# Optimization experiments

Measured on AMD Instinct MI355X. Metric: run time of the kernel, lower is better.

## Reference

```python
import jax, jax.numpy as jnp
import numpy as np

B, L, H, NH, HD, IT = 16, 512, 256, 8, 32, 2
NEG = -9e15


def _ln(x, g, b):
    m = x.mean(-1, keepdims=True)
    v = ((x - m) ** 2).mean(-1, keepdims=True)
    return (x - m) / jnp.sqrt(v + 1e-5) * g + b


def setup_inputs() -> dict:
    key = jax.random.key(0)
    ks = jax.random.split(key, 12)

    def nrm(k, shape, fan_in):
        return jax.random.normal(k, shape, dtype=jnp.float32) / np.float32(np.sqrt(fan_in))

    return {
        "data": jax.random.normal(ks[0], (B, L, H), jnp.float32),
        "gat_WQ_w": nrm(ks[1], (NH, H, H), H),
        "gat_WQ_b": jnp.zeros((NH, H), jnp.float32),
        "gat_a1": nrm(ks[2], (NH, 3 * H), 3 * H),
        "gat_a2": nrm(ks[3], (NH, 3 * H), 3 * H),
        "gat_fc_w": nrm(ks[4], (NH, 3 * H, HD), 3 * H),
        "gat_fc_b": jnp.zeros((NH, HD), jnp.float32),
        "norm_g": jnp.ones((IT, H), jnp.float32),
        "norm_b": jnp.zeros((IT, H), jnp.float32),
        "sq_w": nrm(ks[5], (IT, NH * HD, H), H),
        "sq_b": jnp.zeros((IT, NH * HD), jnp.float32),
        "sk_w": nrm(ks[6], (IT, NH * HD, H), H),
        "sk_b": jnp.zeros((IT, NH * HD), jnp.float32),
        "so_w": nrm(ks[7], (IT, H, NH * HD), NH * HD),
        "so_b": jnp.zeros((IT, H), jnp.float32),
        "fc_w": nrm(ks[8], (NH * HD, H), NH * HD),
        "fc_b": jnp.zeros((H,), jnp.float32),
        "mask": jax.random.randint(ks[9], (B, L), 0, 2, jnp.int32),
        "edge_matrix": jax.random.randint(ks[10], (B, L, L), 0, 2, jnp.int32),
    }


def _gat_head(xn, ax, adj_pos, Wq, bq, a1, a2, Fw, Fb):
    # xn: [B,L,H] normalized nodes; ax: [B,L,2H] interleaved (r_embs, relay)
    h = jnp.concatenate([xn @ Wq.T + bq, ax], axis=-1)  # [B,L,3H]
    # decomposed a^T [h_i ; h_j] = a1.h_i + a2.h_j  (avoids O(N^2*6H) concat)
    ei = h @ a1  # [B,L]
    ej = h @ a2  # [B,L]
    e = jax.nn.leaky_relu(ei[:, :, None] + ej[:, None, :], 0.2)  # [B,L,L]
    att = jax.nn.softmax(jnp.where(adj_pos, e, NEG), axis=2)
    hp = jnp.einsum('bij,bjd->bid', att, h)  # [B,L,3H]
    return jax.nn.elu(hp @ Fw + Fb)  # [B,L,HD]


def _forward(data, gat_WQ_w, gat_WQ_b, gat_a1, gat_a2, gat_fc_w, gat_fc_b,
             norm_g, norm_b, sq_w, sq_b, sk_w, sk_b, so_w, so_b, fc_w, fc_b,
             mask, edge_matrix):
    pad = mask == 0                                   # True at padding positions
    smask = jnp.concatenate([jnp.zeros((B, 1), bool), pad], axis=1)  # [B,L+1]
    adj_pos = edge_matrix > 0
    nodes = data                                      # [B,L,H]
    relay = data.mean(axis=1)                         # [B,H]
    gat = jax.vmap(_gat_head, in_axes=(None, None, None, 0, 0, 0, 0, 0, 0))
    scale = np.float32(1.0 / np.sqrt(HD))

    for i in range(IT):
        xn = _ln(nodes, norm_g[i], norm_b[i])
        # torch views [B,H,2,L] as [B,2H,L]: features interleave (r_embs, relay)
        ax = jnp.stack([data, jnp.broadcast_to(relay[:, None, :], (B, L, H))],
                       axis=-1).reshape(B, L, 2 * H)
        heads = gat(xn, ax, adj_pos, gat_WQ_w, gat_WQ_b, gat_a1, gat_a2,
                    gat_fc_w, gat_fc_b)               # [NH,B,L,HD]
        temp = jnp.transpose(heads, (1, 2, 0, 3)).reshape(B, L, NH * HD)
        nodes = nodes + jax.nn.leaky_relu(temp @ fc_w + fc_b, 0.01)
        # star attention (MSA2); note original uses v = k (WV unused)
        y = jnp.concatenate([relay[:, None, :], nodes], axis=1)   # [B,L+1,H]
        q = (relay @ sq_w[i].T + sq_b[i]).reshape(B, NH, HD)
        k = (y @ sk_w[i].T + sk_b[i]).transpose(0, 2, 1).reshape(B, NH, HD, L + 1)
        v = jnp.swapaxes(k, 2, 3)                                  # [B,NH,L+1,HD]
        pre = jnp.einsum('bnd,bndl->bnl', q, k) * scale
        pre = jnp.where(smask[:, None, :], -jnp.inf, pre)
        al = jax.nn.softmax(pre, axis=2)
        att = jnp.einsum('bnl,bnld->bnd', al, v).reshape(B, NH * HD)
        relay = jax.nn.leaky_relu(att @ so_w[i].T + so_b[i], 0.01)
        nodes = jnp.where(pad[:, :, None], 0.0, nodes)
    return nodes, relay


def reference(data, gat_WQ_w, gat_WQ_b, gat_a1, gat_a2, gat_fc_w, gat_fc_b,
              norm_g, norm_b, sq_w, sq_b, sk_w, sk_b, so_w, so_b, fc_w, fc_b,
              mask, edge_matrix):
    return _forward(data, gat_WQ_w, gat_WQ_b, gat_a1, gat_a2, gat_fc_w, gat_fc_b,
                    norm_g, norm_b, sq_w, sq_b, sk_w, sk_b, so_w, so_b, fc_w, fc_b,
                    mask, edge_matrix)
```

## Files before the change

kernel.cpp:

```cpp
#include <hip/hip_runtime.h>
#include <hip/hip_bf16.h>
#include <math.h>

#define BB 16
#define LL 512
#define HH 256
#define NHEAD 8
#define HDIM 32
#define LP1 513
#define NODES_ELEMS (BB*LL*HH)

typedef __attribute__((ext_vector_type(8))) short bf16x8;
typedef __attribute__((ext_vector_type(4))) float f32x4;

__device__ __forceinline__ unsigned short f2bf(float f) {
  union { float f; unsigned u; } x; x.f = f;
  unsigned r = x.u + 0x7fffu + ((x.u >> 16) & 1u);
  return (unsigned short)(r >> 16);
}
__device__ __forceinline__ float bf2f(unsigned short u) {
  union { unsigned u; float f; } x; x.u = (unsigned)u << 16; return x.f;
}

__global__ __launch_bounds__(256) void mega_prep_kernel(
    const float* __restrict__ data, const int* __restrict__ edge,
    const float* __restrict__ fc_w, const float* __restrict__ fcw,
    const float* __restrict__ sk_w, const float* __restrict__ sq_w,
    const float* __restrict__ so_w, const float* __restrict__ WQw,
    const float* __restrict__ WQb, const float* __restrict__ a1,
    const float* __restrict__ a2,
    unsigned short* __restrict__ datab, unsigned char* __restrict__ ep,
    unsigned short* __restrict__ fcwT, unsigned short* __restrict__ Bcat,
    unsigned short* __restrict__ skwb, float* __restrict__ sqT,
    float* __restrict__ soT, float* __restrict__ rpart,
    float* __restrict__ w1, float* __restrict__ w2,
    float* __restrict__ c1, float* __restrict__ c2,
    float* __restrict__ bqf, float* __restrict__ a1o, float* __restrict__ a2o) {
  __shared__ float smem[64 * 65];
  int blk = blockIdx.x, t = threadIdx.x;
  if (blk < 128) {
    int b = blk >> 3, ch = blk & 7;
    const float* pr = data + ((size_t)b * 512 + ch * 64) * 256 + t;
    unsigned short* db = datab + ((size_t)b * 512 + ch * 64) * 256 + t;
    float s = 0.f;
    for (int l = 0; l < 64; l++) {
      float v = pr[(size_t)l * 256];
      db[(size_t)l * 256] = f2bf(v);
      s += v;
    }
    rpart[(size_t)blk * 256 + t] = s;
  } else if (blk < 2176) {
    int row = (blk - 128) * 4 + (t >> 6);
    int lane = t & 63;
    const int* adj = edge + ((size_t)row << 9) + lane * 8;
    unsigned v = 0;
#pragma unroll
    for (int u = 0; u < 8; u++) v |= (adj[u] > 0 ? 1u : 0u) << u;
    ep[((size_t)row << 6) + lane] = (unsigned char)v;
  } else if (blk < 2432) {
    int idx = (blk - 2176) * 256 + t;
    int d = idx & 31;
    int g = idx >> 5;
    int n = g >> 8, c = g & 255;
    Bcat[((size_t)n * 32 + d) * 512 + 256 + c] =
        f2bf(fcw[((size_t)n * 768 + 256 + 2 * c) * 32 + d]);
  } else if (blk < 2944) {
    int idx = (blk - 2432) * 256 + t;
    skwb[idx] = f2bf(sk_w[idx]);
  } else if (blk < 3024) {
    int q = blk - 2944;
    int mat = q >> 4, tl = q & 15;
    int r0 = (tl >> 2) * 64, c0 = (tl & 3) * 64;
    const float* in;
    if (mat == 0) in = fc_w;
    else if (mat <= 2) in = sq_w + (mat - 1) * 65536;
    else in = so_w + (mat - 3) * 65536;
    int cc = t & 63, rq = t >> 6;
#pragma unroll
    for (int i = 0; i < 16; i++) {
      int r = rq + i * 4;
      smem[r * 65 + cc] = in[(r0 + r) * 256 + c0 + cc];
    }
    __syncthreads();
#pragma unroll
    for (int i = 0; i < 16; i++) {
      int cp = rq + i * 4;
      float v = smem[cc * 65 + cp];
      if (mat == 0) fcwT[(c0 + cp) * 256 + r0 + cc] = f2bf(v);
      else if (mat <= 2) sqT[(mat - 1) * 65536 + (c0 + cp) * 256 + r0 + cc] = v;
      else soT[(mat - 3) * 65536 + (c0 + cp) * 256 + r0 + cc] = v;
    }
  } else if (blk < 3152) {
    int q = blk - 3024;
    int n = q >> 4, kc = q & 15;
    int k = kc * 16 + (t & 15), cseg = t >> 4;
    float s1 = 0.f, s2 = 0.f;
#pragma unroll
    for (int u = 0; u < 16; u++) {
      int c = cseg * 16 + u;
      float wv = WQw[((size_t)(n * 256 + c)) * 256 + k];
      s1 = fmaf(a1[n * 768 + c], wv, s1);
      s2 = fmaf(a2[n * 768 + c], wv, s2);
    }
    smem[cseg * 16 + (t & 15)] = s1;
    smem[256 + cseg * 16 + (t & 15)] = s2;
    __syncthreads();
    if (cseg == 0) {
      float a = 0.f, b2 = 0.f;
#pragma unroll
      for (int u = 0; u < 16; u++) {
        a += smem[u * 16 + (t & 15)];
        b2 += smem[256 + u * 16 + (t & 15)];
      }
      w1[n * 256 + k] = a;
      w2[n * 256 + k] = b2;
    }
  } else if (blk < 3160) {
    int n = blk - 3152;
    int d = t & 31, seg = t >> 5;
    float s = 0.f;
#pragma unroll
    for (int u = 0; u < 32; u++) {
      int c = seg * 32 + u;
      s = fmaf(WQb[n * 256 + c], fcw[((size_t)n * 768 + c) * 32 + d], s);
    }
    smem[seg * 32 + d] = s;
    __syncthreads();
    if (seg == 0) {
      float a = 0.f;
#pragma unroll
      for (int u = 0; u < 8; u++) a += smem[u * 32 + d];
      bqf[n * 32 + d] = a;
    }
  } else if (blk == 3160) {
    int n = t >> 5, sl = t & 31;
    float s1 = 0.f, s2 = 0.f;
#pragma unroll
    for (int u = 0; u < 8; u++) {
      int c = sl * 8 + u;
      float wb = WQb[n * 256 + c];
      s1 = fmaf(a1[n * 768 + c], wb, s1);
      s2 = fmaf(a2[n * 768 + c], wb, s2);
    }
    smem[t] = s1; smem[256 + t] = s2;
    __syncthreads();
    if (sl == 0) {
      float a = 0.f, b2 = 0.f;
      for (int u = 0; u < 32; u++) { a += smem[n * 32 + u]; b2 += smem[256 + n * 32 + u]; }
      c1[n] = a; c2[n] = b2;
    }
  } else {
#pragma unroll
    for (int n = 0; n < 8; n++) {
      a1o[n * 256 + t] = a1[n * 768 + 256 + 2 * t];
      a2o[n * 256 + t] = a2[n * 768 + 256 + 2 * t];
    }
  }
}

__device__ __forceinline__ void rarf_tail(
    int n, int b, int t, const float* rel,
    const float* __restrict__ a1, const float* __restrict__ a2,
    const float* __restrict__ fcw, const float* __restrict__ fcb,
    const float* __restrict__ bqf,
    float* __restrict__ ra1, float* __restrict__ ra2, float* __restrict__ rf,
    float* red1, float* red2, float* pf_s) {
  int lane = t & 63, w = t >> 6;
  float p1 = rel[t] * a1[n * 768 + 257 + 2 * t];
  float p2 = rel[t] * a2[n * 768 + 257 + 2 * t];
#pragma unroll
  for (int o = 32; o; o >>= 1) { p1 += __shfl_xor(p1, o); p2 += __shfl_xor(p2, o); }
  if (lane == 0) { red1[w] = p1; red2[w] = p2; }
  int d = t & 31, seg = t >> 5;
  float pf = 0.f;
  for (int u = 0; u < 32; u++) {
    int k = seg * 32 + u;
    pf = fmaf(rel[k], fcw[((size_t)n * 768 + 257 + 2 * k) * 32 + d], pf);
  }
  pf_s[seg * 33 + d] = pf;
  __syncthreads();
  if (t == 0) {
    ra1[n * 16 + b] = red1[0] + red1[1] + red1[2] + red1[3];
    ra2[n * 16 + b] = red2[0] + red2[1] + red2[2] + red2[3];
  }
  if (t < 32) {
    float s = 0.f;
    for (int gg = 0; gg < 8; gg++) s += pf_s[gg * 33 + t];
    rf[((size_t)n * 16 + b) * 32 + t] = s + fcb[n * 32 + t] + bqf[n * 32 + t];
  }
}

__global__ __launch_bounds__(256) void prep2_kernel(
    const float* __restrict__ WQw, const float* __restrict__ fcw,
    unsigned short* __restrict__ Bcat,
    const float* __restrict__ rpart,
    const unsigned short* __restrict__ skw0, const float* __restrict__ skb0,
    const float* __restrict__ a1, const float* __restrict__ a2,
    const float* __restrict__ fcb, const float* __restrict__ bqf,
    const float* __restrict__ w1, const float* __restrict__ w2,
    const float* __restrict__ a1o, const float* __restrict__ a2o,
    float* __restrict__ relay, unsigned short* __restrict__ ktb,
    float* __restrict__ ra1, float* __restrict__ ra2, float* __restrict__ rf) {
  __shared__ float smem[12288];
  int blk = blockIdx.x, t = threadIdx.x;
  if (blk < 128) {
    float* wq_s = smem;
    float* fw_s = smem + 4096;
    int n = blk >> 4, kt = blk & 15;
#pragma unroll
    for (int i = 0; i < 16; i++) {
      int c = i * 16 + (t >> 4), kk = t & 15;
      wq_s[c * 16 + kk] = WQw[(size_t)n * 65536 + c * 256 + kt * 16 + kk];
    }
#pragma unroll
    for (int i = 0; i < 32; i++) {
      int idx = i * 256 + t;
      fw_s[(idx >> 5) * 32 + (idx & 31)] = fcw[(size_t)n * 24576 + idx];
    }
    __syncthreads();
    int kloc = t >> 4, dp = t & 15;
    float a0 = 0.f, a1v = 0.f;
    for (int c = 0; c < 256; c++) {
      float wv = wq_s[c * 16 + kloc];
      a0 = fmaf(wv, fw_s[c * 32 + dp * 2], a0);
      a1v = fmaf(wv, fw_s[c * 32 + dp * 2 + 1], a1v);
    }
    int k = kt * 16 + kloc;
    Bcat[((size_t)n * 32 + dp * 2) * 512 + k] = f2bf(a0);
    Bcat[((size_t)n * 32 + dp * 2 + 1) * 512 + k] = f2bf(a1v);
  } else if (blk < 256) {
    float* rel = smem;
    float* red1 = smem + 256;
    float* red2 = smem + 264;
    float* pf_s = smem + 272;
    int id = blk - 128;
    int n = id >> 4, b = id & 15;
    float s = 0.f;
#pragma unroll
    for (int ch = 0; ch < 8; ch++) s += rpart[((size_t)(b * 8 + ch)) * 256 + t];
    s *= (1.0f / 512.0f);
    rel[t] = s;
    __syncthreads();
    if (n == 0) {
      relay[b * 256 + t] = s;
      float acc = 0.f;
      for (int k = 0; k < 256; k++) acc = fmaf(rel[k], bf2f(skw0[(size_t)t * 256 + k]), acc);
      ktb[((size_t)b * LP1) * 256 + t] = f2bf(acc + skb0[t]);
    }
    rarf_tail(n, b, t, rel, a1, a2, fcw, fcb, bqf, ra1, ra2, rf, red1, red2, pf_s);
  } else {
    int q = blk - 256;
    int n = q & 7, isEj = q >> 3;
    const float* wsrc = isEj ? w2 : w1;
    const float* asrc = isEj ? a2o : a1o;
#pragma unroll
    for (int h = 0; h < 2; h++) {
      int k = h * 256 + t;
      float v = (k < 256) ? wsrc[n * 256 + k] : asrc[n * 256 + k - 256];
      Bcat[((size_t)(256 + q)) * 512 + k] = f2bf(v);
    }
  }
}

__global__ __launch_bounds__(256) void so_rarf_kernel(
    const float* __restrict__ atts,
    const float* __restrict__ soT_it, const float* __restrict__ sob_it,
    const unsigned short* __restrict__ skw_nx, const float* __restrict__ skb_nx,
    const float* __restrict__ a1, const float* __restrict__ a2,
    const float* __restrict__ fcw, const float* __restrict__ fcb,
    const float* __restrict__ bqf, int do_extras,
    float* __restrict__ relay, unsigned short* __restrict__ ktb,
    float* __restrict__ ra1, float* __restrict__ ra2, float* __restrict__ rf) {
  int n = blockIdx.x >> 4, b = blockIdx.x & 15;
  if (!do_extras && n > 0) return;
  __shared__ float xr[256];
  __shared__ float rel[256];
  __shared__ float red1[4], red2[4];
  __shared__ float pf_s[8 * 33];
  int t = threadIdx.x;
  xr[t] = atts[b * 256 + t];
  __syncthreads();
  float acc = 0.f;
  for (int k = 0; k < 256; k++) acc = fmaf(xr[k], soT_it[(size_t)k * 256 + t], acc);
  float v = acc + sob_it[t];
  v = v > 0.f ? v : 0.01f * v;
  rel[t] = v;
  __syncthreads();
  if (n == 0) relay[b * 256 + t] = v;
  if (!do_extras) return;
  if (n == 0) {
    float a2v = 0.f;
    for (int k = 0; k < 256; k++) a2v = fmaf(rel[k], bf2f(skw_nx[(size_t)t * 256 + k]), a2v);
    ktb[((size_t)b * LP1) * 256 + t] = f2bf(a2v + skb_nx[t]);
  }
  rarf_tail(n, b, t, rel, a1, a2, fcw, fcb, bqf, ra1, ra2, rf, red1, red2, pf_s);
}

__global__ __launch_bounds__(256) void lng_gemm_kernel(
    const float* __restrict__ src,
    const unsigned short* __restrict__ datab,
    const unsigned short* __restrict__ Bcat,
    const float* __restrict__ g, const float* __restrict__ bb,
    const float* __restrict__ c1, const float* __restrict__ c2,
    const float* __restrict__ ra1, const float* __restrict__ ra2,
    unsigned short* __restrict__ GT,
    float* __restrict__ ei, float* __restrict__ ej) {
  __shared__ unsigned short A[32][520];
  int blk = blockIdx.x;
  int b = blk & 15;
  int i0 = (blk >> 4) << 5;
  int t = threadIdx.x;
  int wv = t >> 6, lane = t & 63;
  int lo = lane & 15, quad = lane >> 4;

  float4 g4 = *(const float4*)(g + lane * 4);
  float4 b4 = *(const float4*)(bb + lane * 4);
  float xs[8][4];
  float sum[8], sq[8];
#pragma unroll
  for (int rr = 0; rr < 8; rr++) {
    int grow = b * 512 + i0 + wv * 8 + rr;
    float4 v = *(const float4*)(src + (size_t)grow * 256 + lane * 4);
    xs[rr][0] = v.x; xs[rr][1] = v.y; xs[rr][2] = v.z; xs[rr][3] = v.w;
    sum[rr] = v.x + v.y + v.z + v.w;
    sq[rr] = v.x * v.x + v.y * v.y + v.z * v.z + v.w * v.w;
    ushort4 dv4 = *(const ushort4*)(datab + (size_t)grow * 256 + lane * 4);
    *(ushort4*)&A[wv * 8 + rr][256 + lane * 4] = dv4;
  }
#pragma unroll
  for (int o = 32; o; o >>= 1) {
#pragma unroll
    for (int rr = 0; rr < 8; rr++) {
      sum[rr] += __shfl_xor(sum[rr], o);
      sq[rr] += __shfl_xor(sq[rr], o);
    }
  }
#pragma unroll
  for (int rr = 0; rr < 8; rr++) {
    float mean = sum[rr] * (1.0f / 256.0f);
    float var = sq[rr] * (1.0f / 256.0f) - mean * mean;
    float rstd = rsqrtf(var + 1e-5f);
    ushort4 pk;
    pk.x = f2bf((xs[rr][0] - mean) * rstd * g4.x + b4.x);
    pk.y = f2bf((xs[rr][1] - mean) * rstd * g4.y + b4.y);
    pk.z = f2bf((xs[rr][2] - mean) * rstd * g4.z + b4.z);
    pk.w = f2bf((xs[rr][3] - mean) * rstd * g4.w + b4.w);
    *(ushort4*)&A[wv * 8 + rr][lane * 4] = pk;
  }
  __syncthreads();

  f32x4 acc[2][4] = {};
  f32x4 acce[2] = {};
  for (int k0 = 0; k0 < 512; k0 += 32) {
    bf16x8 af[2];
#pragma unroll
    for (int rt = 0; rt < 2; rt++)
      af[rt] = *(const bf16x8*)&A[rt * 16 + lo][k0 + quad * 8];
#pragma unroll
    for (int j = 0; j < 4; j++) {
      int tile = j * 4 + wv;
      bf16x8 bf_ = *(const bf16x8*)(Bcat + (size_t)(tile * 16 + lo) * 512 + k0 + quad * 8);
#pragma unroll
      for (int rt = 0; rt < 2; rt++)
        acc[rt][j] = __builtin_amdgcn_mfma_f32_16x16x32_bf16(af[rt], bf_, acc[rt][j], 0, 0, 0);
    }
    if (wv == 0) {
      bf16x8 bf_ = *(const bf16x8*)(Bcat + (size_t)(256 + lo) * 512 + k0 + quad * 8);
#pragma unroll
      for (int rt = 0; rt < 2; rt++)
        acce[rt] = __builtin_amdgcn_mfma_f32_16x16x32_bf16(af[rt], bf_, acce[rt], 0, 0, 0);
    }
  }
#pragma unroll
  for (int j = 0; j < 4; j++) {
    int tile = j * 4 + wv;
    int co = tile * 16 + lo;
    int n = co >> 5, d = co & 31;
#pragma unroll
    for (int rt = 0; rt < 2; rt++) {
      int jj = i0 + rt * 16 + quad * 4;
      ushort4 pk;
      pk.x = f2bf(acc[rt][j][0]);
      pk.y = f2bf(acc[rt][j][1]);
      pk.z = f2bf(acc[rt][j][2]);
      pk.w = f2bf(acc[rt][j][3]);
      *(ushort4*)&GT[(((size_t)(n * 16 + b) * 32 + d) << 9) + jj] = pk;
    }
  }
  if (wv == 0) {
    int n = lo & 7, isEj = lo >> 3;
    float cst = isEj ? (c2[n] + ra2[n * 16 + b]) : (c1[n] + ra1[n * 16 + b]);
    float* outp = isEj ? ej : ei;
#pragma unroll
    for (int rt = 0; rt < 2; rt++) {
#pragma unroll
      for (int r = 0; r < 4; r++) {
        int row = i0 + rt * 16 + quad * 4 + r;
        outp[n * 8192 + b * 512 + row] = acce[rt][r] + cst;
      }
    }
  }
}

__global__ __launch_bounds__(256) void gat_agg_kernel(
    const unsigned short* __restrict__ GT,
    const float* __restrict__ ei, const float* __restrict__ ej,
    const unsigned char* __restrict__ ep,
    const float* __restrict__ rf,
    unsigned short* __restrict__ tempb) {
  __shared__ unsigned short W[32][512];
  __shared__ float denom_s[32];
  int blk = blockIdx.x;
  int sib = blk >> 7;
  int g = blk & 127;
  int n = g >> 4;
  int b = g & 15;
  int i0 = sib << 5;
  int t = threadIdx.x;
  int wv = t >> 6, lane = t & 63;
  int lo = lane & 15, quad = lane >> 4;

  const float* ejrow = ej + n * 8192 + b * 512;
  float ejv[8];
  {
    float4 e0 = *(const float4*)(ejrow + lane * 8);
    float4 e1 = *(const float4*)(ejrow + lane * 8 + 4);
    ejv[0] = e0.x; ejv[1] = e0.y; ejv[2] = e0.z; ejv[3] = e0.w;
    ejv[4] = e1.x; ejv[5] = e1.y; ejv[6] = e1.z; ejv[7] = e1.w;
  }
  float mm = ejv[0];
#pragma unroll
  for (int u = 1; u < 8; u++) mm = fmaxf(mm, ejv[u]);
#pragma unroll
  for (int o = 32; o; o >>= 1) mm = fmaxf(mm, __shfl_xor(mm, o));

  for (int rr = 0; rr < 8; rr++) {
    int row = wv * 8 + rr;
    float eiv = ei[n * 8192 + b * 512 + i0 + row];
    float M = eiv + mm;
    M = M > 0.f ? M : 0.2f * M;
    unsigned pbv = ep[(((size_t)(b * 512 + i0 + row)) << 6) + lane];
    bf16x8 wpack;
#pragma unroll
    for (int u = 0; u < 8; u++) {
      float e = eiv + ejv[u];
      e = e > 0.f ? e : 0.2f * e;
      float w = ((pbv >> u) & 1) ? __expf(e - M) : 0.f;
      wpack[u] = (short)f2bf(w);
    }
    *(bf16x8*)&W[row][(lane ^ (row & 7)) << 3] = wpack;
  }
  __syncthreads();

  int rt = wv >> 1, dh = wv & 1;
  int arow = rt * 16 + lo;
  int rx = arow & 7;
  const unsigned short* gtb = GT + (((size_t)(n * 16 + b) * 32) << 9);
  bf16x8 bones;
  {
    short ov = (lo == 0) ? (short)0x3F80 : (short)0;
#pragma unroll
    for (int j = 0; j < 8; j++) bones[j] = ov;
  }
  f32x4 acc = {}, accd = {};
  for (int k0 = 0; k0 < 512; k0 += 32) {
    int chunk = (k0 >> 3) + quad;
    bf16x8 a0 = *(const bf16x8*)&W[arow][(chunk ^ rx) << 3];
    bf16x8 bf_ = *(const bf16x8*)(gtb + (((size_t)(dh * 16 + lo)) << 9) + k0 + quad * 8);
    acc = __builtin_amdgcn_mfma_f32_16x16x32_bf16(a0, bf_, acc, 0, 0, 0);
    if (dh == 0)
      accd = __builtin_amdgcn_mfma_f32_16x16x32_bf16(a0, bones, accd, 0, 0, 0);
  }
  if (dh == 0 && lo == 0) {
#pragma unroll
    for (int r = 0; r < 4; r++) denom_s[rt * 16 + quad * 4 + r] = accd[r];
  }
  __syncthreads();
  int d = dh * 16 + lo;
  float base = rf[((size_t)n * 16 + b) * 32 + d];
#pragma unroll
  for (int r = 0; r < 4; r++) {
    int row = rt * 16 + quad * 4 + r;
    float inv = 1.0f / fmaxf(denom_s[row], 1e-35f);
    float v = acc[r] * inv + base;
    v = v > 0.f ? v : expm1f(v);
    tempb[((size_t)(b * 512 + i0 + row)) * 256 + n * 32 + d] = f2bf(v);
  }
}

__global__ __launch_bounds__(256) void fc_kt_kernel(
    const unsigned short* __restrict__ tempb,
    const unsigned short* __restrict__ fcwT,
    const float* __restrict__ fc_b,
    const unsigned short* __restrict__ skw_it,
    const float* __restrict__ skb_it,
    const int* __restrict__ mask,
    const float* __restrict__ resid,
    float* __restrict__ nodes,
    unsigned short* __restrict__ ktb) {
  __shared__ unsigned short tmp[32][264];
  int blk = blockIdx.x;
  int b = blk & 15;
  int i0 = (blk >> 4) << 5;
  int t = threadIdx.x;
  int wv = t >> 6, lane = t & 63;
  int lo = lane & 15, quad = lane >> 4;
  int ch = wv >> 1, rt2 = wv & 1;

  const unsigned short* arow_p = tempb + ((size_t)(b * 512 + i0 + rt2 * 16 + lo)) * 256 + quad * 8;
  f32x4 facc[8] = {};
  for (int k0 = 0; k0 < 256; k0 += 32) {
    bf16x8 a0 = *(const bf16x8*)(arow_p + k0);
#pragma unroll
    for (int ct = 0; ct < 8; ct++) {
      int co = ch * 128 + ct * 16 + lo;
      bf16x8 bf_ = *(const bf16x8*)(fcwT + (size_t)co * 256 + k0 + quad * 8);
      facc[ct] = __builtin_amdgcn_mfma_f32_16x16x32_bf16(a0, bf_, facc[ct], 0, 0, 0);
    }
  }
#pragma unroll
  for (int ct = 0; ct < 8; ct++) {
    int co = ch * 128 + ct * 16 + lo;
    float bv = fc_b[co];
#pragma unroll
    for (int r = 0; r < 4; r++) {
      int row = rt2 * 16 + quad * 4 + r;
      int grow = b * 512 + i0 + row;
      float v = facc[ct][r] + bv;
      v = v > 0.f ? v : 0.01f * v;
      v = (mask[grow] != 0) ? resid[(size_t)grow * 256 + co] + v : 0.f;
      nodes[(size_t)grow * 256 + co] = v;
      tmp[row][co] = f2bf(v);
    }
  }
  __syncthreads();

  f32x4 kacc[8] = {};
  for (int k0 = 0; k0 < 256; k0 += 32) {
    bf16x8 a0 = *(const bf16x8*)&tmp[rt2 * 16 + lo][k0 + quad * 8];
#pragma unroll
    for (int ct = 0; ct < 8; ct++) {
      int co = ch * 128 + ct * 16 + lo;
      bf16x8 bf_ = *(const bf16x8*)(skw_it + (size_t)co * 256 + k0 + quad * 8);
      kacc[ct] = __builtin_amdgcn_mfma_f32_16x16x32_bf16(a0, bf_, kacc[ct], 0, 0, 0);
    }
  }
#pragma unroll
  for (int ct = 0; ct < 8; ct++) {
    int co = ch * 128 + ct * 16 + lo;
    float bv = skb_it[co];
#pragma unroll
    for (int r = 0; r < 4; r++) {
      int row = rt2 * 16 + quad * 4 + r;
      int yrow = b * LP1 + 1 + i0 + row;
      ktb[(size_t)yrow * 256 + co] = f2bf(kacc[ct][r] + bv);
    }
  }
}

__global__ __launch_bounds__(256) void star_attn_kernel(const float* __restrict__ relay,
                                                        const float* __restrict__ sqT_it,
                                                        const float* __restrict__ sqb_it,
                                                        const unsigned short* __restrict__ ktb,
                                                        const int* __restrict__ mask,
                                                        float* __restrict__ attstar) {
  int n = blockIdx.x >> 4, b = blockIdx.x & 15;
  int t = threadIdx.x;
  int lane = t & 63, w = t >> 6;
  __shared__ float relb[256];
  __shared__ float qv[32];
  __shared__ float pre[LP1];
  __shared__ float red[4];
  __shared__ float par[8][33];
  relb[t] = relay[b * 256 + t];
  __syncthreads();
  {
    int d = t & 31, g = t >> 5;
    float qp = 0.f;
    for (int k = 0; k < 32; k++)
      qp = fmaf(relb[g * 32 + k], sqT_it[(size_t)(g * 32 + k) * 256 + n * 32 + d], qp);
    par[g][d] = qp;
  }
  __syncthreads();
  if (t < 32) {
    float q = 0.f;
#pragma unroll
    for (int gg = 0; gg < 8; gg++) q += par[gg][t];
    qv[t] = q + sqb_it[n * 32 + t];
  }
  __syncthreads();
  const float scale = 0.17677669529663687f;
  for (int l = t; l < LP1; l += 256) {
    bool masked = (l > 0) && (mask[b * LL + l - 1] == 0);
    float p;
    if (masked) p = -3.4e38f;
    else {
      p = 0.f;
      const bf16x8* krow8 = (const bf16x8*)(ktb + ((size_t)b * LP1 + l) * 256 + n * 32);
#pragma unroll
      for (int dd = 0; dd < 4; dd++) {
        bf16x8 kv = krow8[dd];
#pragma unroll
        for (int j = 0; j < 8; j++)
          p = fmaf(qv[dd * 8 + j], bf2f((unsigned short)kv[j]), p);
      }
      p *= scale;
    }
    pre[l] = p;
  }
  __syncthreads();
  float m = -3.4e38f;
  for (int l = t; l < LP1; l += 256) m = fmaxf(m, pre[l]);
#pragma unroll
  for (int o = 32; o; o >>= 1) m = fmaxf(m, __shfl_xor(m, o));
  if (lane == 0) red[w] = m;
  __syncthreads();
  m = fmaxf(fmaxf(red[0], red[1]), fmaxf(red[2], red[3]));
  __syncthreads();
  float s = 0.f;
  for (int l = t; l < LP1; l += 256) {
    float wv = __expf(pre[l] - m);
    pre[l] = wv;
    s += wv;
  }
#pragma unroll
  for (int o = 32; o; o >>= 1) s += __shfl_xor(s, o);
  if (lane == 0) red[w] = s;
  __syncthreads();
  float denom = red[0] + red[1] + red[2] + red[3];
  int d = t & 31, g = t >> 5;
  float acc = 0.f;
  for (int l = g; l < LP1; l += 8)
    acc = fmaf(pre[l], bf2f(ktb[((size_t)b * LP1 + l) * 256 + n * 32 + d]), acc);
  par[g][d] = acc;
  __syncthreads();
  if (t < 32) {
    float a = 0.f;
    for (int gg = 0; gg < 8; gg++) a += par[gg][t];
    attstar[b * 256 + n * 32 + t] = a / denom;
  }
}

extern "C" void kernel_launch(void* const* d_in, const int* in_sizes, int n_in,
                              void* d_out, int out_size, void* d_ws, size_t ws_size,
                              hipStream_t stream) {
  const float* data  = (const float*)d_in[0];
  const float* WQw   = (const float*)d_in[1];
  const float* WQb   = (const float*)d_in[2];
  const float* a1    = (const float*)d_in[3];
  const float* a2    = (const float*)d_in[4];
  const float* fcw_g = (const float*)d_in[5];
  const float* fcb_g = (const float*)d_in[6];
  const float* ng    = (const float*)d_in[7];
  const float* nb    = (const float*)d_in[8];
  const float* sq_w  = (const float*)d_in[9];
  const float* sq_b  = (const float*)d_in[10];
  const float* sk_w  = (const float*)d_in[11];
  const float* sk_b  = (const float*)d_in[12];
  const float* so_w  = (const float*)d_in[13];
  const float* so_b  = (const float*)d_in[14];
  const float* fc_w  = (const float*)d_in[15];
  const float* fc_b  = (const float*)d_in[16];
  const int*   mask  = (const int*)d_in[17];
  const int*   edge  = (const int*)d_in[18];

  float* nodes = (float*)d_out;
  float* relay = nodes + NODES_ELEMS;

  char* p = (char*)d_ws;
  auto alloc = [&](size_t bytes) -> char* {
    char* r = p; p += (bytes + 255) & ~(size_t)255; return r;
  };
  unsigned short* datab= (unsigned short*)alloc((size_t)8192 * 256 * 2);
  unsigned short* GT   = (unsigned short*)alloc((size_t)8 * 16 * 32 * 512 * 2);
  unsigned short* tmpb = (unsigned short*)alloc((size_t)8192 * 256 * 2);
  unsigned short* ktb  = (unsigned short*)alloc((size_t)8208 * 256 * 2);
  unsigned char* ep    = (unsigned char*)alloc((size_t)8192 * 64);
  float* ei            = (float*)alloc(65536 * 4);
  float* ej            = (float*)alloc(65536 * 4);
  float* ra1           = (float*)alloc(128 * 4);
  float* ra2           = (float*)alloc(128 * 4);
  float* rf            = (float*)alloc(4096 * 4);
  float* bqf           = (float*)alloc(256 * 4);
  float* w1            = (float*)alloc(2048 * 4);
  float* w2            = (float*)alloc(2048 * 4);
  float* c1            = (float*)alloc(8 * 4);
  float* c2            = (float*)alloc(8 * 4);
  float* a1o           = (float*)alloc(2048 * 4);
  float* a2o           = (float*)alloc(2048 * 4);
  float* rpart         = (float*)alloc(128 * 256 * 4);
  unsigned short* Bcat = (unsigned short*)alloc((size_t)288 * 512 * 2);
  unsigned short* fcwT = (unsigned short*)alloc((size_t)65536 * 2);
  unsigned short* skwb = (unsigned short*)alloc((size_t)131072 * 2);
  float* sqT           = (float*)alloc((size_t)131072 * 4);
  float* soT           = (float*)alloc((size_t)131072 * 4);
  float* atts          = (float*)alloc(4096 * 4);

  mega_prep_kernel<<<3162, 256, 0, stream>>>(data, edge, fc_w, fcw_g, sk_w, sq_w,
                                             so_w, WQw, WQb, a1, a2,
                                             datab, ep, fcwT, Bcat, skwb, sqT, soT,
                                             rpart, w1, w2, c1, c2, bqf, a1o, a2o);
  prep2_kernel<<<272, 256, 0, stream>>>(WQw, fcw_g, Bcat, rpart, skwb, sk_b,
                                        a1, a2, fcb_g, bqf, w1, w2, a1o, a2o,
                                        relay, ktb, ra1, ra2, rf);

  for (int it = 0; it < 2; it++) {
    const float* src = (it == 0) ? data : nodes;
    lng_gemm_kernel<<<256, 256, 0, stream>>>(src, datab, Bcat,
                                             ng + it * 256, nb + it * 256,
                                             c1, c2, ra1, ra2, GT, ei, ej);
    gat_agg_kernel<<<NHEAD * BB * 16, 256, 0, stream>>>(GT, ei, ej, ep, rf, tmpb);
    fc_kt_kernel<<<256, 256, 0, stream>>>(tmpb, fcwT, fc_b,
                                          skwb + it * 65536, sk_b + it * 256,
                                          mask, src, nodes, ktb);
    star_attn_kernel<<<BB * NHEAD, 256, 0, stream>>>(relay, sqT + it * 65536,
                                                     sq_b + it * 256, ktb, mask, atts);
    so_rarf_kernel<<<128, 256, 0, stream>>>(atts, soT + it * 65536, so_b + it * 256,
                                            skwb + 65536, sk_b + 256,
                                            a1, a2, fcw_g, fcb_g, bqf,
                                            (it == 0) ? 1 : 0,
                                            relay, ktb, ra1, ra2, rf);
  }
}
```

Baseline: 322.1 us.

## Fuse relay update into next iteration's LN-GEMM kernel prologue

Removes the separate so_rarf kernel between iterations. Its work (relay output projection, relay key row, GAT relay attention and fc terms) now runs redundantly in every lng_gemm block when post is set, and only the i0==0 blocks write relay, ktb and rf. A small relay_final kernel computes the last relay after the loop. This saves one launch per iteration but adds redundant per-block matvecs (256x256 soT plus fc weights) to a kernel that runs 256 blocks, and it relies on gat_agg reading rf only after lng_gemm has finished.

```diff
diff --git a/kernel.cpp b/kernel.cpp
--- a/kernel.cpp
+++ b/kernel.cpp
@@ -262,38 +262,18 @@
   }
 }
 
-__global__ __launch_bounds__(256) void so_rarf_kernel(
+__global__ __launch_bounds__(256) void relay_final_kernel(
     const float* __restrict__ atts,
     const float* __restrict__ soT_it, const float* __restrict__ sob_it,
-    const unsigned short* __restrict__ skw_nx, const float* __restrict__ skb_nx,
-    const float* __restrict__ a1, const float* __restrict__ a2,
-    const float* __restrict__ fcw, const float* __restrict__ fcb,
-    const float* __restrict__ bqf, int do_extras,
-    float* __restrict__ relay, unsigned short* __restrict__ ktb,
-    float* __restrict__ ra1, float* __restrict__ ra2, float* __restrict__ rf) {
-  int n = blockIdx.x >> 4, b = blockIdx.x & 15;
-  if (!do_extras && n > 0) return;
+    float* __restrict__ relay) {
   __shared__ float xr[256];
-  __shared__ float rel[256];
-  __shared__ float red1[4], red2[4];
-  __shared__ float pf_s[8 * 33];
-  int t = threadIdx.x;
+  int b = blockIdx.x, t = threadIdx.x;
   xr[t] = atts[b * 256 + t];
   __syncthreads();
   float acc = 0.f;
   for (int k = 0; k < 256; k++) acc = fmaf(xr[k], soT_it[(size_t)k * 256 + t], acc);
   float v = acc + sob_it[t];
-  v = v > 0.f ? v : 0.01f * v;
-  rel[t] = v;
-  __syncthreads();
-  if (n == 0) relay[b * 256 + t] = v;
-  if (!do_extras) return;
-  if (n == 0) {
-    float a2v = 0.f;
-    for (int k = 0; k < 256; k++) a2v = fmaf(rel[k], bf2f(skw_nx[(size_t)t * 256 + k]), a2v);
-    ktb[((size_t)b * LP1) * 256 + t] = f2bf(a2v + skb_nx[t]);
-  }
-  rarf_tail(n, b, t, rel, a1, a2, fcw, fcb, bqf, ra1, ra2, rf, red1, red2, pf_s);
+  relay[b * 256 + t] = v > 0.f ? v : 0.01f * v;
 }
 
 __global__ __launch_bounds__(256) void lng_gemm_kernel(
@@ -303,15 +283,73 @@
     const float* __restrict__ g, const float* __restrict__ bb,
     const float* __restrict__ c1, const float* __restrict__ c2,
     const float* __restrict__ ra1, const float* __restrict__ ra2,
+    int post,
+    const float* __restrict__ atts,
+    const float* __restrict__ soT_pre, const float* __restrict__ sob_pre,
+    const unsigned short* __restrict__ skw_it, const float* __restrict__ skb_it,
+    const float* __restrict__ a1, const float* __restrict__ a2,
+    const float* __restrict__ fcw, const float* __restrict__ fcb,
+    const float* __restrict__ bqf,
+    float* __restrict__ relay, unsigned short* __restrict__ ktb,
+    float* __restrict__ rf,
     unsigned short* __restrict__ GT,
     float* __restrict__ ei, float* __restrict__ ej) {
   __shared__ unsigned short A[32][520];
+  __shared__ float xr_s[256];
+  __shared__ float rel_s[256];
+  __shared__ float pr_s[256];
+  __shared__ float ra_s[16];
   int blk = blockIdx.x;
   int b = blk & 15;
   int i0 = (blk >> 4) << 5;
   int t = threadIdx.x;
   int wv = t >> 6, lane = t & 63;
   int lo = lane & 15, quad = lane >> 4;
+
+  if (post) {
+    xr_s[t] = atts[b * 256 + t];
+    __syncthreads();
+    float acc = 0.f;
+    for (int k = 0; k < 256; k++) acc = fmaf(xr_s[k], soT_pre[(size_t)k * 256 + t], acc);
+    float v = acc + sob_pre[t];
+    v = v > 0.f ? v : 0.01f * v;
+    rel_s[t] = v;
+    __syncthreads();
+    if (i0 == 0) {
+      relay[b * 256 + t] = v;
+      float kk = 0.f;
+      for (int k = 0; k < 256; k++) kk = fmaf(rel_s[k], bf2f(skw_it[(size_t)t * 256 + k]), kk);
+      ktb[((size_t)b * LP1) * 256 + t] = f2bf(kk + skb_it[t]);
+    }
+    {
+      int nn = t >> 5, sl = t & 31;
+      float p1 = 0.f, p2 = 0.f;
+#pragma unroll
+      for (int u = 0; u < 8; u++) {
+        int k = sl * 8 + u;
+        p1 = fmaf(rel_s[k], a1[nn * 768 + 257 + 2 * k], p1);
+        p2 = fmaf(rel_s[k], a2[nn * 768 + 257 + 2 * k], p2);
+      }
+      xr_s[t] = p1; pr_s[t] = p2;
+    }
+    __syncthreads();
+    if ((t & 31) == 0) {
+      int nn = t >> 5;
+      float s1 = 0.f, s2 = 0.f;
+#pragma unroll
+      for (int u = 0; u < 32; u++) { s1 += xr_s[t + u]; s2 += pr_s[t + u]; }
+      ra_s[nn] = s1; ra_s[8 + nn] = s2;
+    }
+    {
+      int nn = t >> 5, d = t & 31;
+      float s = 0.f;
+      for (int k = 0; k < 256; k++)
+        s = fmaf(rel_s[k], fcw[((size_t)nn * 768 + 257 + 2 * k) * 32 + d], s);
+      s += fcb[nn * 32 + d] + bqf[nn * 32 + d];
+      if (i0 == 0) rf[((size_t)nn * 16 + b) * 32 + d] = s;
+    }
+    __syncthreads();
+  }
 
   float4 g4 = *(const float4*)(g + lane * 4);
   float4 b4 = *(const float4*)(bb + lane * 4);
@@ -389,7 +427,9 @@
   }
   if (wv == 0) {
     int n = lo & 7, isEj = lo >> 3;
-    float cst = isEj ? (c2[n] + ra2[n * 16 + b]) : (c1[n] + ra1[n * 16 + b]);
+    float rav = post ? ra_s[isEj * 8 + n]
+                     : (isEj ? ra2[n * 16 + b] : ra1[n * 16 + b]);
+    float cst = (isEj ? c2[n] : c1[n]) + rav;
     float* outp = isEj ? ej : ei;
 #pragma unroll
     for (int rt = 0; rt < 2; rt++) {
@@ -708,17 +748,19 @@
     const float* src = (it == 0) ? data : nodes;
     lng_gemm_kernel<<<256, 256, 0, stream>>>(src, datab, Bcat,
                                              ng + it * 256, nb + it * 256,
-                                             c1, c2, ra1, ra2, GT, ei, ej);
+                                             c1, c2, ra1, ra2,
+                                             it,
+                                             atts, soT, so_b,
+                                             skwb + 65536, sk_b + 256,
+                                             a1, a2, fcw_g, fcb_g, bqf,
+                                             relay, ktb, rf,
+                                             GT, ei, ej);
     gat_agg_kernel<<<NHEAD * BB * 16, 256, 0, stream>>>(GT, ei, ej, ep, rf, tmpb);
     fc_kt_kernel<<<256, 256, 0, stream>>>(tmpb, fcwT, fc_b,
                                           skwb + it * 65536, sk_b + it * 256,
                                           mask, src, nodes, ktb);
     star_attn_kernel<<<BB * NHEAD, 256, 0, stream>>>(relay, sqT + it * 65536,
                                                      sq_b + it * 256, ktb, mask, atts);
-    so_rarf_kernel<<<128, 256, 0, stream>>>(atts, soT + it * 65536, so_b + it * 256,
-                                            skwb + 65536, sk_b + 256,
-                                            a1, a2, fcw_g, fcb_g, bqf,
-                                            (it == 0) ? 1 : 0,
-                                            relay, ktb, ra1, ra2, rf);
-  }
-}
+  }
+  relay_final_kernel<<<BB, 256, 0, stream>>>(atts, soT + 65536, so_b + 256, relay);
+}
```

After: 323.6 us. About the same (+0.5%).
